# Kernel tuning notes

Hardware: AMD Instinct MI355X
Metric: run time of the kernel (lower is better)

Reference implementation:

```python
import jax, jax.numpy as jnp
import numpy as np

B, T, D = 2, 2048, 1024
H = 16
HD = D // H  # 64
A = 16
MLP_H = 4 * D
EPS = 1e-6


def rmsnorm(x, w):
    # x: [..., C], w: [C]
    return x * jax.lax.rsqrt(jnp.mean(x * x, axis=-1, keepdims=True) + EPS) * w


def setup_inputs() -> dict:
    key = jax.random.key(0)
    ks = jax.random.split(key, 24)
    s = 0.02
    inp = {
        'x': jax.random.normal(ks[0], (B, T, D), jnp.float32),
        'actions': jax.random.normal(ks[1], (B, T, A), jnp.float32),
        # block norms
        'n1_w': jnp.ones((D,), jnp.float32),
        'n2_w': jnp.ones((D,), jnp.float32),
        # attention projections (stored [in, out])
        'q_w': jax.random.normal(ks[2], (D, D), jnp.float32) * s,
        'q_b': jnp.zeros((D,), jnp.float32),
        'k_w': jax.random.normal(ks[3], (D, D), jnp.float32) * s,
        'k_b': jnp.zeros((D,), jnp.float32),
        'v_w': jax.random.normal(ks[4], (D, D), jnp.float32) * s,
        'v_b': jnp.zeros((D,), jnp.float32),
        'qn_w': jnp.ones((HD,), jnp.float32),
        'kn_w': jnp.ones((HD,), jnp.float32),
        'o_w': jax.random.normal(ks[5], (D, D), jnp.float32) * s,
        'o_b': jnp.zeros((D,), jnp.float32),
        # action conditioning
        'ae1_w': jax.random.normal(ks[6], (A, D), jnp.float32) * s,
        'ae1_b': jnp.zeros((D,), jnp.float32),
        'ae2_w': jax.random.normal(ks[7], (D, D), jnp.float32) * s,
        'ae2_b': jnp.zeros((D,), jnp.float32),
        'mod_w': jax.random.normal(ks[8], (D, 4 * D), jnp.float32) * s,
        'mod_b': jnp.zeros((4 * D,), jnp.float32),
        # mlp
        'm1_w': jax.random.normal(ks[9], (D, MLP_H), jnp.float32) * s,
        'm1_b': jnp.zeros((MLP_H,), jnp.float32),
        'm2_w': jax.random.normal(ks[10], (MLP_H, D), jnp.float32) * s,
        'm2_b': jnp.zeros((D,), jnp.float32),
    }
    return inp


def _forward(x, actions, n1_w, n2_w, q_w, q_b, k_w, k_b, v_w, v_b, qn_w, kn_w,
             o_w, o_b, ae1_w, ae1_b, ae2_w, ae2_b, mod_w, mod_b,
             m1_w, m1_b, m2_w, m2_b):
    Bc, Tc, Dc = x.shape
    scale = HD ** -0.5

    # --- causal temporal attention with QK RMSNorm ---
    h = rmsnorm(x, n1_w)
    q = (h @ q_w + q_b).reshape(Bc, Tc, H, HD).transpose(0, 2, 1, 3)  # [B,H,T,hd]
    k = (h @ k_w + k_b).reshape(Bc, Tc, H, HD).transpose(0, 2, 1, 3)
    v = (h @ v_w + v_b).reshape(Bc, Tc, H, HD).transpose(0, 2, 1, 3)
    q = rmsnorm(q, qn_w)
    k = rmsnorm(k, kn_w)
    attn = jnp.einsum('bhqd,bhkd->bhqk', q, k) * scale
    causal = jnp.triu(jnp.ones((Tc, Tc), bool), k=1)  # True above diagonal -> masked
    attn = jnp.where(causal, -jnp.inf, attn)
    attn = jax.nn.softmax(attn, axis=-1)
    out = jnp.einsum('bhqk,bhkd->bhqd', attn, v)
    out = out.transpose(0, 2, 1, 3).reshape(Bc, Tc, Dc)
    x = x + (out @ o_w + o_b)

    # --- action conditioning (AdaLN-style; eval mode, no dropout) ---
    ae = jax.nn.silu(actions @ ae1_w + ae1_b) @ ae2_w + ae2_b  # [B,T,D]
    mod = jax.nn.silu(ae) @ mod_w + mod_b  # [B,T,4D]
    shift1, scale1, _, _ = jnp.split(mod, 4, axis=-1)
    x = x * (1.0 + scale1) + shift1

    # --- MLP ---
    h2 = rmsnorm(x, n2_w)
    x = x + (jax.nn.gelu(h2 @ m1_w + m1_b, approximate=False) @ m2_w + m2_b)
    return x


def reference(x, actions, n1_w, n2_w, q_w, q_b, k_w, k_b, v_w, v_b, qn_w, kn_w,
              o_w, o_b, ae1_w, ae1_b, ae2_w, ae2_b, mod_w, mod_b,
              m1_w, m1_b, m2_w, m2_b):
    return _forward(x, actions, n1_w, n2_w, q_w, q_b, k_w, k_b, v_w, v_b,
                    qn_w, kn_w, o_w, o_b, ae1_w, ae1_b, ae2_w, ae2_b,
                    mod_w, mod_b, m1_w, m1_b, m2_w, m2_b)
```

## Files before the change

kernel.cpp:

```cpp
#include <hip/hip_runtime.h>
#include <hip/hip_bf16.h>
#include <math.h>

typedef __hip_bfloat16 bf16;
typedef __attribute__((ext_vector_type(8))) short short8;
typedef __attribute__((ext_vector_type(4))) float float4_;

#define B_   2
#define T_   2048
#define D_   1024
#define H_   16
#define NTOK (B_ * T_)
#define NEG_SENT -1e30f

#define AS1 __attribute__((address_space(1)))
#define AS3 __attribute__((address_space(3)))

static __device__ __forceinline__ float b2f(bf16 v) { return __bfloat162float(v); }
static __device__ __forceinline__ bf16  f2b(float v) { return __float2bfloat16(v); }
static __device__ __forceinline__ short f2s(float v) {
    unsigned u = __builtin_bit_cast(unsigned, v);
    unsigned r = (u + 0x7FFFu + ((u >> 16) & 1u)) >> 16;
    return (short)r;
}
static __device__ __forceinline__ float to_f(float v) { return v; }
static __device__ __forceinline__ float to_f(bf16 v) { return __bfloat162float(v); }
static __device__ __forceinline__ void  store_o(float* p, float v) { *p = v; }
static __device__ __forceinline__ void  store_o(bf16* p, float v) { *p = __float2bfloat16(v); }
static __device__ __forceinline__ void gl_lds16(const void* g, void* l) {
    __builtin_amdgcn_global_load_lds((const AS1 unsigned int*)g, (AS3 unsigned int*)l, 16, 0, 0);
}

__global__ __launch_bounds__(256) void rmsnorm_k(const float* __restrict__ x,
                                                 const float* __restrict__ w,
                                                 bf16* __restrict__ out) {
    int t = blockIdx.x, tid = threadIdx.x;
    float xs[4], ss = 0.f;
#pragma unroll
    for (int i = 0; i < 4; ++i) {
        float v = x[(size_t)t * D_ + tid + i * 256];
        xs[i] = v; ss += v * v;
    }
    __shared__ float red[4];
#pragma unroll
    for (int off = 32; off > 0; off >>= 1) ss += __shfl_xor(ss, off, 64);
    if ((tid & 63) == 0) red[tid >> 6] = ss;
    __syncthreads();
    ss = red[0] + red[1] + red[2] + red[3];
    float inv = rsqrtf(ss * (1.f / D_) + 1e-6f);
#pragma unroll
    for (int i = 0; i < 4; ++i) {
        int c = tid + i * 256;
        out[(size_t)t * D_ + c] = f2b(xs[i] * inv * w[c]);
    }
}

__global__ __launch_bounds__(256) void modnorm_k(float* __restrict__ x1,
                                                 const bf16* __restrict__ mod,
                                                 const float* __restrict__ w,
                                                 bf16* __restrict__ h2) {
    int t = blockIdx.x, tid = threadIdx.x;
    float xs[4], ss = 0.f;
#pragma unroll
    for (int i = 0; i < 4; ++i) {
        int c = tid + i * 256;
        float sh = b2f(mod[(size_t)t * 2048 + c]);
        float sc = b2f(mod[(size_t)t * 2048 + 1024 + c]);
        float v = x1[(size_t)t * D_ + c] * (1.f + sc) + sh;
        xs[i] = v; ss += v * v;
        x1[(size_t)t * D_ + c] = v;
    }
    __shared__ float red[4];
#pragma unroll
    for (int off = 32; off > 0; off >>= 1) ss += __shfl_xor(ss, off, 64);
    if ((tid & 63) == 0) red[tid >> 6] = ss;
    __syncthreads();
    ss = red[0] + red[1] + red[2] + red[3];
    float inv = rsqrtf(ss * (1.f / D_) + 1e-6f);
#pragma unroll
    for (int i = 0; i < 4; ++i) {
        int c = tid + i * 256;
        h2[(size_t)t * D_ + c] = f2b(xs[i] * inv * w[c]);
    }
}

__global__ __launch_bounds__(256) void ae1_k(const float* __restrict__ actions,
                                             const float* __restrict__ w,
                                             const float* __restrict__ b,
                                             bf16* __restrict__ out) {
    int t = blockIdx.x, tid = threadIdx.x;
    float av[16];
#pragma unroll
    for (int a = 0; a < 16; ++a) av[a] = actions[(size_t)t * 16 + a];
#pragma unroll
    for (int i = 0; i < 4; ++i) {
        int n = tid + i * 256;
        float acc = b[n];
#pragma unroll
        for (int a = 0; a < 16; ++a) acc += av[a] * w[a * D_ + n];
        out[(size_t)t * D_ + n] = f2b(acc / (1.f + expf(-acc)));
    }
}

struct WD { const float* src; bf16* dst; int K, N, ldw, tiles; };
struct WPack { WD d[8]; };
__global__ __launch_bounds__(256) void wprep_k(WPack p) {
    int bid = blockIdx.x;
    int mi = 0, cum = 0;
#pragma unroll
    for (mi = 0; mi < 8; ++mi) {
        if (bid < cum + p.d[mi].tiles) break;
        cum += p.d[mi].tiles;
    }
    if (mi >= 8) return;
    WD w = p.d[mi];
    int local = bid - cum;
    int tilesK = w.K >> 6;
    int tk = local % tilesK, tn = local / tilesK;
    int k0 = tk * 64, n0 = tn * 64;
    __shared__ short Tt[64 * 72];
    int t = threadIdx.x;
    int row = t >> 2, seg = t & 3;
    const float* sp = w.src + (size_t)(k0 + row) * w.ldw + n0 + seg * 16;
#pragma unroll
    for (int q = 0; q < 4; ++q) {
        float4_ f = *(const float4_*)(sp + q * 4);
#pragma unroll
        for (int j = 0; j < 4; ++j) Tt[(seg * 16 + q * 4 + j) * 72 + row] = f2s(f[j]);
    }
    __syncthreads();
    bf16* dp = w.dst + (size_t)(n0 + row) * w.K + k0 + seg * 16;
    *(short8*)dp       = *(const short8*)&Tt[row * 72 + seg * 16];
    *(short8*)(dp + 8) = *(const short8*)&Tt[row * 72 + seg * 16 + 8];
}

__global__ __launch_bounds__(256) void bcat_k(const float* __restrict__ qb,
                                              const float* __restrict__ kb,
                                              const float* __restrict__ vb,
                                              float* __restrict__ dst) {
    int i = blockIdx.x * 256 + threadIdx.x;
    const float* s = (i < 1024) ? qb : (i < 2048) ? kb : vb;
    dst[i] = s[i & 1023];
}

template <int ACT, int QKN, typename ResT, typename OutT>
__global__ __launch_bounds__(256) void gemm_k(const bf16* __restrict__ A,
                                              const bf16* __restrict__ Bt,
                                              const float* __restrict__ bias,
                                              const ResT* __restrict__ res,
                                              OutT* __restrict__ out,
                                              int M, int N, int K, int ldo,
                                              const float* __restrict__ qn_w,
                                              const float* __restrict__ kn_w) {
    __shared__ __align__(16) short As[128 * 64];
    __shared__ __align__(16) short Bs[128 * 64];
    const int tid = threadIdx.x;
    const int bm = blockIdx.y * 128, bn = blockIdx.x * 128;
    const int wave = tid >> 6, lane = tid & 63;
    const int wm = (wave & 1) * 64, wn = (wave >> 1) * 64;
    const int l15 = lane & 15, quad = lane >> 4;
    const int lrow = lane >> 3, lseg = (lane & 7) * 8;
    float4_ acc[4][4] = {};

    for (int k0 = 0; k0 < K; k0 += 64) {
#pragma unroll
        for (int it = 0; it < 4; ++it) {
            int r = it * 32 + wave * 8;
            gl_lds16((const short*)A + (size_t)(bm + r + lrow) * K + k0 + lseg, &As[r * 64]);
            gl_lds16((const short*)Bt + (size_t)(bn + r + lrow) * K + k0 + lseg, &Bs[r * 64]);
        }
        __syncthreads();
#pragma unroll
        for (int kk = 0; kk < 64; kk += 32) {
            short8 af[4], bfr[4];
#pragma unroll
            for (int i = 0; i < 4; ++i)
                af[i] = *(const short8*)&As[(wm + i * 16 + l15) * 64 + kk + quad * 8];
#pragma unroll
            for (int j = 0; j < 4; ++j)
                bfr[j] = *(const short8*)&Bs[(wn + j * 16 + l15) * 64 + kk + quad * 8];
#pragma unroll
            for (int i = 0; i < 4; ++i)
#pragma unroll
                for (int j = 0; j < 4; ++j)
                    acc[i][j] = __builtin_amdgcn_mfma_f32_16x16x32_bf16(af[i], bfr[j], acc[i][j], 0, 0, 0);
        }
        __syncthreads();
    }

    int seg = (bn + wn) >> 10;
    float nwv[4];
    if (QKN && seg < 2) {
        const float* nw = seg ? kn_w : qn_w;
#pragma unroll
        for (int j = 0; j < 4; ++j) nwv[j] = nw[j * 16 + l15];
    }

#pragma unroll
    for (int i = 0; i < 4; ++i) {
        float vv[4][4];
#pragma unroll
        for (int j = 0; j < 4; ++j) {
            float bv = bias[bn + wn + j * 16 + l15];
#pragma unroll
            for (int r = 0; r < 4; ++r) vv[j][r] = acc[i][j][r] + bv;
        }
        if (QKN && seg < 2) {
#pragma unroll
            for (int r = 0; r < 4; ++r) {
                float ss = vv[0][r] * vv[0][r] + vv[1][r] * vv[1][r]
                         + vv[2][r] * vv[2][r] + vv[3][r] * vv[3][r];
#pragma unroll
                for (int off = 8; off > 0; off >>= 1) ss += __shfl_xor(ss, off, 16);
                float inv = rsqrtf(ss * (1.f / 64.f) + 1e-6f);
#pragma unroll
                for (int j = 0; j < 4; ++j) vv[j][r] *= inv * nwv[j];
            }
        }
#pragma unroll
        for (int j = 0; j < 4; ++j) {
            int col = bn + wn + j * 16 + l15;
#pragma unroll
            for (int r = 0; r < 4; ++r) {
                int row = bm + wm + i * 16 + quad * 4 + r;
                float v = vv[j][r];
                if (ACT == 1) v = v / (1.f + expf(-v));
                else if (ACT == 2) v = 0.5f * v * (1.f + erff(v * 0.70710678118654752f));
                if (res) v += to_f(res[(size_t)row * ldo + col]);
                store_o(&out[(size_t)row * ldo + col], v);
            }
        }
    }
}

template <int ACT, typename ResT, typename OutT>
__global__ __launch_bounds__(256) void gemm64_k(const bf16* __restrict__ A,
                                                const bf16* __restrict__ Bt,
                                                const float* __restrict__ bias,
                                                const ResT* __restrict__ res,
                                                OutT* __restrict__ out,
                                                int M, int N, int K) {
    __shared__ __align__(16) short As[64 * 64];
    __shared__ __align__(16) short Bs[128 * 64];
    const int tid = threadIdx.x;
    const int bm = blockIdx.y * 64, bn = blockIdx.x * 128;
    const int wave = tid >> 6, lane = tid & 63;
    const int wm = (wave & 1) * 32, wn = (wave >> 1) * 64;
    const int l15 = lane & 15, quad = lane >> 4;
    const int lrow = lane >> 3, lseg = (lane & 7) * 8;
    float4_ acc[2][4] = {};

    for (int k0 = 0; k0 < K; k0 += 64) {
#pragma unroll
        for (int it = 0; it < 2; ++it) {
            int r = wave * 16 + it * 8;
            gl_lds16((const short*)A + (size_t)(bm + r + lrow) * K + k0 + lseg, &As[r * 64]);
        }
#pragma unroll
        for (int it = 0; it < 4; ++it) {
            int r = it * 32 + wave * 8;
            gl_lds16((const short*)Bt + (size_t)(bn + r + lrow) * K + k0 + lseg, &Bs[r * 64]);
        }
        __syncthreads();
#pragma unroll
        for (int kk = 0; kk < 64; kk += 32) {
            short8 af[2], bfr[4];
#pragma unroll
            for (int i = 0; i < 2; ++i)
                af[i] = *(const short8*)&As[(wm + i * 16 + l15) * 64 + kk + quad * 8];
#pragma unroll
            for (int j = 0; j < 4; ++j)
                bfr[j] = *(const short8*)&Bs[(wn + j * 16 + l15) * 64 + kk + quad * 8];
#pragma unroll
            for (int i = 0; i < 2; ++i)
#pragma unroll
                for (int j = 0; j < 4; ++j)
                    acc[i][j] = __builtin_amdgcn_mfma_f32_16x16x32_bf16(af[i], bfr[j], acc[i][j], 0, 0, 0);
        }
        __syncthreads();
    }

#pragma unroll
    for (int i = 0; i < 2; ++i)
#pragma unroll
        for (int j = 0; j < 4; ++j) {
            int col = bn + wn + j * 16 + l15;
            float bv = bias[col];
#pragma unroll
            for (int r = 0; r < 4; ++r) {
                int row = bm + wm + i * 16 + quad * 4 + r;
                float v = acc[i][j][r] + bv;
                if (ACT == 1) v = v / (1.f + expf(-v));
                else if (ACT == 2) v = 0.5f * v * (1.f + erff(v * 0.70710678118654752f));
                if (res) v += to_f(res[(size_t)row * N + col]);
                store_o(&out[(size_t)row * N + col], v);
            }
        }
}

__global__ __launch_bounds__(256) void attn_k(const bf16* __restrict__ QKV,
                                              bf16* __restrict__ O) {
    __shared__ __align__(16) short Vt[2][64 * 72];
    __shared__ __align__(16) short Ps[4][16 * 72];
    const int bh = blockIdx.y, b = bh >> 4, h = bh & 15;
    const int q0 = T_ - 64 * (blockIdx.x + 1);
    const int tid = threadIdx.x, wave = tid >> 6, lane = tid & 63;
    const int l15 = lane & 15, quad = lane >> 4;
    const size_t base = (size_t)b * T_ * 3072 + h * 64;
    const short* Qp = (const short*)QKV + base;
    const short* Kp = Qp + 1024;
    const short* Vp = Qp + 2048;

    const int qrow = q0 + wave * 16 + l15;
    short8 qf0 = *(const short8*)(Qp + (size_t)qrow * 3072 + quad * 8);
    short8 qf1 = *(const short8*)(Qp + (size_t)qrow * 3072 + 32 + quad * 8);

    float4_ oacc[4] = {};
    float l_r[4] = {0.f, 0.f, 0.f, 0.f};

    const int vrow = tid >> 2, vseg = tid & 3;
    const int nit = q0 / 64 + 1;

    {
        const short* vp = Vp + (size_t)vrow * 3072 + vseg * 16;
        short8 v0 = *(const short8*)vp;
        short8 v1 = *(const short8*)(vp + 8);
#pragma unroll
        for (int j = 0; j < 8; ++j) Vt[0][(vseg * 16 + j) * 72 + vrow] = v0[j];
#pragma unroll
        for (int j = 0; j < 8; ++j) Vt[0][(vseg * 16 + 8 + j) * 72 + vrow] = v1[j];
    }
    __syncthreads();

    for (int it = 0; it < nit; ++it) {
        const int kv0 = it * 64, buf = it & 1;
        if (it + 1 < nit) {
            const short* vp = Vp + (size_t)(kv0 + 64 + vrow) * 3072 + vseg * 16;
            short8 v0 = *(const short8*)vp;
            short8 v1 = *(const short8*)(vp + 8);
#pragma unroll
            for (int j = 0; j < 8; ++j) Vt[buf ^ 1][(vseg * 16 + j) * 72 + vrow] = v0[j];
#pragma unroll
            for (int j = 0; j < 8; ++j) Vt[buf ^ 1][(vseg * 16 + 8 + j) * 72 + vrow] = v1[j];
        }

        float4_ s[4];
#pragma unroll
        for (int c = 0; c < 4; ++c) {
            const short* kp = Kp + (size_t)(kv0 + c * 16 + l15) * 3072 + quad * 8;
            short8 kb0 = *(const short8*)kp;
            short8 kb1 = *(const short8*)(kp + 32);
            float4_ sc = {};
            sc = __builtin_amdgcn_mfma_f32_16x16x32_bf16(qf0, kb0, sc, 0, 0, 0);
            sc = __builtin_amdgcn_mfma_f32_16x16x32_bf16(qf1, kb1, sc, 0, 0, 0);
            s[c] = sc;
        }

#pragma unroll
        for (int r = 0; r < 4; ++r) {
            int qr = q0 + wave * 16 + quad * 4 + r;
#pragma unroll
            for (int c = 0; c < 4; ++c) {
                int kvi = kv0 + c * 16 + l15;
                float val = (kvi > qr) ? NEG_SENT : s[c][r] * 0.125f;
                float p = __expf(val);
                s[c][r] = p;
                l_r[r] += p;
            }
        }

#pragma unroll
        for (int c = 0; c < 4; ++c)
#pragma unroll
            for (int r = 0; r < 4; ++r)
                Ps[wave][(quad * 4 + r) * 72 + c * 16 + l15] = f2s(s[c][r]);

#pragma unroll
        for (int kk = 0; kk < 64; kk += 32) {
            short8 pf = *(const short8*)&Ps[wave][l15 * 72 + kk + quad * 8];
#pragma unroll
            for (int d = 0; d < 4; ++d) {
                short8 vf = *(const short8*)&Vt[buf][(d * 16 + l15) * 72 + kk + quad * 8];
                oacc[d] = __builtin_amdgcn_mfma_f32_16x16x32_bf16(pf, vf, oacc[d], 0, 0, 0);
            }
        }
        __syncthreads();
    }

    float linv[4];
#pragma unroll
    for (int r = 0; r < 4; ++r) {
        float l = l_r[r];
#pragma unroll
        for (int off = 8; off > 0; off >>= 1) l += __shfl_xor(l, off, 16);
        linv[r] = 1.f / l;
    }
#pragma unroll
    for (int d = 0; d < 4; ++d)
#pragma unroll
        for (int r = 0; r < 4; ++r) {
            int qr = q0 + wave * 16 + quad * 4 + r;
            O[(size_t)(b * T_ + qr) * D_ + h * 64 + d * 16 + l15] = f2b(oacc[d][r] * linv[r]);
        }
}

extern "C" void kernel_launch(void* const* d_in, const int* in_sizes, int n_in,
                              void* d_out, int out_size, void* d_ws, size_t ws_size,
                              hipStream_t stream) {
    const float* x     = (const float*)d_in[0];
    const float* acts  = (const float*)d_in[1];
    const float* n1_w  = (const float*)d_in[2];
    const float* n2_w  = (const float*)d_in[3];
    const float* q_w   = (const float*)d_in[4];
    const float* q_b   = (const float*)d_in[5];
    const float* k_w   = (const float*)d_in[6];
    const float* k_b   = (const float*)d_in[7];
    const float* v_w   = (const float*)d_in[8];
    const float* v_b   = (const float*)d_in[9];
    const float* qn_w  = (const float*)d_in[10];
    const float* kn_w  = (const float*)d_in[11];
    const float* o_w   = (const float*)d_in[12];
    const float* o_b   = (const float*)d_in[13];
    const float* ae1_w = (const float*)d_in[14];
    const float* ae1_b = (const float*)d_in[15];
    const float* ae2_w = (const float*)d_in[16];
    const float* ae2_b = (const float*)d_in[17];
    const float* mod_w = (const float*)d_in[18];
    const float* mod_b = (const float*)d_in[19];
    const float* m1_w  = (const float*)d_in[20];
    const float* m1_b  = (const float*)d_in[21];
    const float* m2_w  = (const float*)d_in[22];
    const float* m2_b  = (const float*)d_in[23];
    float* out = (float*)d_out;

    char* ws = (char*)d_ws;
    const size_t MB = 1ull << 20;
    bf16*  Ah   = (bf16*)(ws + 0);
    bf16*  QKVp = (bf16*)(ws + 8 * MB);
    bf16*  AO   = (bf16*)(ws + 32 * MB);
    bf16*  AE1  = (bf16*)(ws + 8 * MB);
    bf16*  AES  = (bf16*)(ws + 16 * MB);
    bf16*  MOD  = (bf16*)(ws + 24 * MB);
    bf16*  M1G  = (bf16*)(ws + 8 * MB);
    float* X1   = out;

    bf16* WTqkv = (bf16*)(ws + 40 * MB);
    bf16* WTo   = (bf16*)(ws + 46 * MB);
    bf16* WTae2 = (bf16*)(ws + 48 * MB);
    bf16* WTmod = (bf16*)(ws + 50 * MB);
    bf16* WTm1  = (bf16*)(ws + 54 * MB);
    bf16* WTm2  = (bf16*)(ws + 62 * MB);
    float* biasQKV = (float*)(ws + 70 * MB);

    dim3 blk(256);

    WPack p;
    p.d[0] = { q_w,   WTqkv,                1024, 1024, 1024, 256 };
    p.d[1] = { k_w,   WTqkv + 1024 * 1024,  1024, 1024, 1024, 256 };
    p.d[2] = { v_w,   WTqkv + 2048 * 1024,  1024, 1024, 1024, 256 };
    p.d[3] = { o_w,   WTo,   1024, 1024, 1024, 256 };
    p.d[4] = { ae2_w, WTae2, 1024, 1024, 1024, 256 };
    p.d[5] = { mod_w, WTmod, 1024, 2048, 4096, 512 };
    p.d[6] = { m1_w,  WTm1,  1024, 4096, 4096, 1024 };
    p.d[7] = { m2_w,  WTm2,  4096, 1024, 1024, 1024 };
    wprep_k<<<3840, blk, 0, stream>>>(p);
    bcat_k<<<12, blk, 0, stream>>>(q_b, k_b, v_b, biasQKV);

    rmsnorm_k<<<NTOK, blk, 0, stream>>>(x, n1_w, Ah);
    gemm_k<0, 1, float, bf16><<<dim3(24, 32), blk, 0, stream>>>(Ah, WTqkv, biasQKV, (const float*)nullptr, QKVp, NTOK, 3072, 1024, 3072, qn_w, kn_w);
    attn_k<<<dim3(T_ / 64, B_ * H_), blk, 0, stream>>>(QKVp, AO);
    gemm64_k<0, float, float><<<dim3(8, 64), blk, 0, stream>>>(AO, WTo, o_b, x, X1, NTOK, 1024, 1024);
    ae1_k<<<NTOK, blk, 0, stream>>>(acts, ae1_w, ae1_b, AE1);
    gemm64_k<1, float, bf16><<<dim3(8, 64), blk, 0, stream>>>(AE1, WTae2, ae2_b, (const float*)nullptr, AES, NTOK, 1024, 1024);
    gemm_k<0, 0, float, bf16><<<dim3(16, 32), blk, 0, stream>>>(AES, WTmod, mod_b, (const float*)nullptr, MOD, NTOK, 2048, 1024, 2048, nullptr, nullptr);
    modnorm_k<<<NTOK, blk, 0, stream>>>(X1, MOD, n2_w, Ah);
    gemm_k<2, 0, float, bf16><<<dim3(32, 32), blk, 0, stream>>>(Ah, WTm1, m1_b, (const float*)nullptr, M1G, NTOK, 4096, 1024, 4096, nullptr, nullptr);
    gemm64_k<0, float, float><<<dim3(8, 64), blk, 0, stream>>>(M1G, WTm2, m2_b, X1, out, NTOK, 1024, 4096);
}
```

Baseline: 596.5 us.

## Split causal attention KV range across blocks and fold softmax scale into Q

Long causal query blocks now have their key/value range split into up to four chunks, each handled by its own block. A new combine kernel sums the unnormalized partial outputs and row sums, which works because no running max is used. The goal is to balance work across the causal triangle and give the GPU more blocks. The 1/sqrt(d)*log2(e) scale moves into the Q norm weights, so the attention loop uses exp2 with no multiply, masks after the exp, and packs P to bf16 with v_cvt_pk_bf16_f32. The cost is extra workspace, fp32 partial traffic and one more launch, and the split path is only taken when the workspace is large enough.

Result: faster. 558.8 us (-6.3%).

```diff
diff --git a/kernel.cpp b/kernel.cpp
--- a/kernel.cpp
+++ b/kernel.cpp
@@ -11,7 +11,7 @@
 #define D_   1024
 #define H_   16
 #define NTOK (B_ * T_)
-#define NEG_SENT -1e30f
+#define QSCALE 0.18033688011112042f
 
 #define AS1 __attribute__((address_space(1)))
 #define AS3 __attribute__((address_space(3)))
@@ -192,8 +192,9 @@
     float nwv[4];
     if (QKN && seg < 2) {
         const float* nw = seg ? kn_w : qn_w;
-#pragma unroll
-        for (int j = 0; j < 4; ++j) nwv[j] = nw[j * 16 + l15];
+        float qsc = seg ? 1.f : QSCALE;
+#pragma unroll
+        for (int j = 0; j < 4; ++j) nwv[j] = nw[j * 16 + l15] * qsc;
     }
 
 #pragma unroll
@@ -298,12 +299,34 @@
         }
 }
 
+static __device__ __forceinline__ int chunk_base(int qb) {
+    return (qb < 16) ? (qb - 8) * 2
+         : (qb < 24) ? 16 + (qb - 16) * 3
+                     : 40 + (qb - 24) * 4;
+}
+
+template <int SPLIT>
 __global__ __launch_bounds__(256) void attn_k(const bf16* __restrict__ QKV,
-                                              bf16* __restrict__ O) {
+                                              bf16* __restrict__ O,
+                                              float* __restrict__ OP,
+                                              float* __restrict__ LP) {
     __shared__ __align__(16) short Vt[2][64 * 72];
     __shared__ __align__(16) short Ps[4][16 * 72];
     const int bh = blockIdx.y, b = bh >> 4, h = bh & 15;
-    const int q0 = T_ - 64 * (blockIdx.x + 1);
+    int qb, ci;
+    if (SPLIT) {
+        int idx = 79 - (int)blockIdx.x;
+        if (idx < 8)       { qb = idx; ci = 0; }
+        else if (idx < 24) { qb = 8 + ((idx - 8) >> 1); ci = (idx - 8) & 1; }
+        else if (idx < 48) { int u = idx - 24; int q3 = u / 3; qb = 16 + q3; ci = u - q3 * 3; }
+        else               { int u = idx - 48; qb = 24 + (u >> 2); ci = u & 3; }
+    } else { qb = 31 - (int)blockIdx.x; ci = 0; }
+    const int n   = qb + 1;
+    const int nc  = SPLIT ? ((qb >> 3) + 1) : 1;
+    const int bsz = n / nc, rem = n - bsz * nc;
+    const int t0  = ci * bsz + (ci < rem ? ci : rem);
+    const int t1  = t0 + bsz + (ci < rem ? 1 : 0);
+    const int q0  = qb * 64;
     const int tid = threadIdx.x, wave = tid >> 6, lane = tid & 63;
     const int l15 = lane & 15, quad = lane >> 4;
     const size_t base = (size_t)b * T_ * 3072 + h * 64;
@@ -319,10 +342,9 @@
     float l_r[4] = {0.f, 0.f, 0.f, 0.f};
 
     const int vrow = tid >> 2, vseg = tid & 3;
-    const int nit = q0 / 64 + 1;
 
     {
-        const short* vp = Vp + (size_t)vrow * 3072 + vseg * 16;
+        const short* vp = Vp + (size_t)(t0 * 64 + vrow) * 3072 + vseg * 16;
         short8 v0 = *(const short8*)vp;
         short8 v1 = *(const short8*)(vp + 8);
 #pragma unroll
@@ -332,10 +354,10 @@
     }
     __syncthreads();
 
-    for (int it = 0; it < nit; ++it) {
-        const int kv0 = it * 64, buf = it & 1;
-        if (it + 1 < nit) {
-            const short* vp = Vp + (size_t)(kv0 + 64 + vrow) * 3072 + vseg * 16;
+    for (int t = t0; t < t1; ++t) {
+        const int kv0 = t * 64, buf = (t - t0) & 1;
+        if (t + 1 < t1) {
+            const short* vp = Vp + (size_t)((t + 1) * 64 + vrow) * 3072 + vseg * 16;
             short8 v0 = *(const short8*)vp;
             short8 v1 = *(const short8*)(vp + 8);
 #pragma unroll
@@ -356,24 +378,41 @@
             s[c] = sc;
         }
 
-#pragma unroll
-        for (int r = 0; r < 4; ++r) {
-            int qr = q0 + wave * 16 + quad * 4 + r;
-#pragma unroll
-            for (int c = 0; c < 4; ++c) {
-                int kvi = kv0 + c * 16 + l15;
-                float val = (kvi > qr) ? NEG_SENT : s[c][r] * 0.125f;
-                float p = __expf(val);
-                s[c][r] = p;
-                l_r[r] += p;
+        if (t == qb) {
+#pragma unroll
+            for (int r = 0; r < 4; ++r) {
+                int qr = q0 + wave * 16 + quad * 4 + r;
+#pragma unroll
+                for (int c = 0; c < 4; ++c) {
+                    int kvi = kv0 + c * 16 + l15;
+                    float p = __builtin_amdgcn_exp2f(s[c][r]);
+                    p = (kvi > qr) ? 0.f : p;
+                    s[c][r] = p;
+                    l_r[r] += p;
+                }
             }
-        }
-
-#pragma unroll
-        for (int c = 0; c < 4; ++c)
+        } else {
 #pragma unroll
             for (int r = 0; r < 4; ++r)
-                Ps[wave][(quad * 4 + r) * 72 + c * 16 + l15] = f2s(s[c][r]);
+#pragma unroll
+                for (int c = 0; c < 4; ++c) {
+                    float p = __builtin_amdgcn_exp2f(s[c][r]);
+                    s[c][r] = p;
+                    l_r[r] += p;
+                }
+        }
+
+#pragma unroll
+        for (int c = 0; c < 4; ++c) {
+            int pk01, pk23;
+            asm("v_cvt_pk_bf16_f32 %0, %1, %2" : "=v"(pk01) : "v"(s[c][0]), "v"(s[c][1]));
+            asm("v_cvt_pk_bf16_f32 %0, %1, %2" : "=v"(pk23) : "v"(s[c][2]), "v"(s[c][3]));
+            short* pp = &Ps[wave][(quad * 4) * 72 + c * 16 + l15];
+            pp[0]   = (short)pk01;
+            pp[72]  = (short)(((unsigned)pk01) >> 16);
+            pp[144] = (short)pk23;
+            pp[216] = (short)(((unsigned)pk23) >> 16);
+        }
 
 #pragma unroll
         for (int kk = 0; kk < 64; kk += 32) {
@@ -387,21 +426,74 @@
         __syncthreads();
     }
 
-    float linv[4];
+    float lsum[4];
 #pragma unroll
     for (int r = 0; r < 4; ++r) {
         float l = l_r[r];
 #pragma unroll
         for (int off = 8; off > 0; off >>= 1) l += __shfl_xor(l, off, 16);
-        linv[r] = 1.f / l;
-    }
-#pragma unroll
-    for (int d = 0; d < 4; ++d)
-#pragma unroll
-        for (int r = 0; r < 4; ++r) {
-            int qr = q0 + wave * 16 + quad * 4 + r;
-            O[(size_t)(b * T_ + qr) * D_ + h * 64 + d * 16 + l15] = f2b(oacc[d][r] * linv[r]);
-        }
+        lsum[r] = l;
+    }
+
+    if (!SPLIT || nc == 1) {
+#pragma unroll
+        for (int d = 0; d < 4; ++d)
+#pragma unroll
+            for (int r = 0; r < 4; ++r) {
+                int qr = q0 + wave * 16 + quad * 4 + r;
+                O[(size_t)(b * T_ + qr) * D_ + h * 64 + d * 16 + l15] = f2b(oacc[d][r] / lsum[r]);
+            }
+    } else {
+        const int slot = bh * 72 + chunk_base(qb) + ci;
+        float* op = OP + (size_t)slot * 4096;
+#pragma unroll
+        for (int d = 0; d < 4; ++d)
+#pragma unroll
+            for (int r = 0; r < 4; ++r)
+                op[(wave * 16 + quad * 4 + r) * 64 + d * 16 + l15] = oacc[d][r];
+        if (l15 == 0) {
+#pragma unroll
+            for (int r = 0; r < 4; ++r)
+                LP[slot * 64 + wave * 16 + quad * 4 + r] = lsum[r];
+        }
+    }
+}
+
+__global__ __launch_bounds__(256) void comb_k(const float* __restrict__ OP,
+                                              const float* __restrict__ LP,
+                                              bf16* __restrict__ O) {
+    const int qb = 8 + (int)blockIdx.x;
+    const int bh = blockIdx.y, b = bh >> 4, h = bh & 15;
+    const int nc = (qb >> 3) + 1;
+    const int slot0 = bh * 72 + chunk_base(qb);
+    const int tid = threadIdx.x;
+    const int row = tid >> 2, c0 = (tid & 3) << 4;
+    const float* p = OP + (size_t)slot0 * 4096 + row * 64 + c0;
+    float4_ a0 = *(const float4_*)(p + 0);
+    float4_ a1 = *(const float4_*)(p + 4);
+    float4_ a2 = *(const float4_*)(p + 8);
+    float4_ a3 = *(const float4_*)(p + 12);
+    float l = LP[slot0 * 64 + row];
+    for (int c = 1; c < nc; ++c) {
+        const float* q = p + (size_t)c * 4096;
+        a0 += *(const float4_*)(q + 0);
+        a1 += *(const float4_*)(q + 4);
+        a2 += *(const float4_*)(q + 8);
+        a3 += *(const float4_*)(q + 12);
+        l += LP[(slot0 + c) * 64 + row];
+    }
+    float inv = 1.f / l;
+    short8 w0, w1;
+#pragma unroll
+    for (int j = 0; j < 4; ++j) {
+        w0[j]     = f2s(a0[j] * inv);
+        w0[4 + j] = f2s(a1[j] * inv);
+        w1[j]     = f2s(a2[j] * inv);
+        w1[4 + j] = f2s(a3[j] * inv);
+    }
+    bf16* o = O + (size_t)(b * T_ + qb * 64 + row) * D_ + h * 64 + c0;
+    *(short8*)o       = w0;
+    *(short8*)(o + 8) = w1;
 }
 
 extern "C" void kernel_launch(void* const* d_in, const int* in_sizes, int n_in,
@@ -451,6 +543,9 @@
     bf16* WTm1  = (bf16*)(ws + 54 * MB);
     bf16* WTm2  = (bf16*)(ws + 62 * MB);
     float* biasQKV = (float*)(ws + 70 * MB);
+    float* OPART = (float*)(ws + 70 * MB + 16384);
+    float* LPART = (float*)(ws + 70 * MB + 16384 + 37748736);
+    const bool split = ws_size >= (70 * MB + 16384 + 37748736ull + 589824ull);
 
     dim3 blk(256);
 
@@ -468,7 +563,12 @@
 
     rmsnorm_k<<<NTOK, blk, 0, stream>>>(x, n1_w, Ah);
     gemm_k<0, 1, float, bf16><<<dim3(24, 32), blk, 0, stream>>>(Ah, WTqkv, biasQKV, (const float*)nullptr, QKVp, NTOK, 3072, 1024, 3072, qn_w, kn_w);
-    attn_k<<<dim3(T_ / 64, B_ * H_), blk, 0, stream>>>(QKVp, AO);
+    if (split) {
+        attn_k<1><<<dim3(80, B_ * H_), blk, 0, stream>>>(QKVp, AO, OPART, LPART);
+        comb_k<<<dim3(24, B_ * H_), blk, 0, stream>>>(OPART, LPART, AO);
+    } else {
+        attn_k<0><<<dim3(32, B_ * H_), blk, 0, stream>>>(QKVp, AO, OPART, LPART);
+    }
     gemm64_k<0, float, float><<<dim3(8, 64), blk, 0, stream>>>(AO, WTo, o_b, x, X1, NTOK, 1024, 1024);
     ae1_k<<<NTOK, blk, 0, stream>>>(acts, ae1_w, ae1_b, AE1);
     gemm64_k<1, float, bf16><<<dim3(8, 64), blk, 0, stream>>>(AE1, WTae2, ae2_b, (const float*)nullptr, AES, NTOK, 1024, 1024);
```
